# Kernel optimization log

Hardware: AMD Instinct MI355X
Metric: run time of the kernel (lower is better)

## Reference

```python
import jax, jax.numpy as jnp
import numpy as np

NUM_HEADS = 8  # from init_kwargs


def setup_inputs() -> dict:
    key = jax.random.key(0)
    ks = jax.random.split(key, 6)
    B, C, H, W = 16, 512, 64, 64
    ctx_dim = 256
    return {
        "x": jax.random.normal(ks[0], (B, C, H, W), dtype=jnp.float32),
        "context": jax.random.normal(ks[1], (B, ctx_dim), dtype=jnp.float32),
        "Wq": jax.random.normal(ks[2], (C, C), dtype=jnp.float32) * 0.02,
        "Wkv": jax.random.normal(ks[3], (2 * C, ctx_dim), dtype=jnp.float32) * 0.02,
        "Wout": jax.random.normal(ks[4], (C, C), dtype=jnp.float32) * 0.02,
        "bout": jax.random.normal(ks[5], (C,), dtype=jnp.float32) * 0.02,
    }


def reference(x, context, Wq, Wkv, Wout, bout):
    # x: [B, C, H, W], context: [B, ctx_dim]; single KV token cross-attention.
    B, C, H, W = x.shape
    N = H * W
    h = NUM_HEADS
    hd = C // h
    scale = hd ** -0.5

    xq = x.reshape(B, C, N).transpose(0, 2, 1)        # [B, N, C]
    q = xq @ Wq.T                                      # [B, N, C]
    kv = context @ Wkv.T                               # [B, 2C]
    k, v = kv[:, :C], kv[:, C:]                        # [B, C] each

    qh = q.reshape(B, N, h, hd)                        # [B, N, h, hd]
    kh = k.reshape(B, h, hd)                           # [B, h, hd] (single token)
    vh = v.reshape(B, h, hd)                           # [B, h, hd]

    # scores over a single KV token -> softmax over size-1 axis is all ones,
    # but we keep the faithful math as the correctness baseline.
    logits = jnp.einsum('bnhd,bhd->bnh', qh, kh) * scale   # [B, N, h]
    attn = jax.nn.softmax(logits[..., None], axis=-1)      # [B, N, h, 1]
    out = attn * vh[:, None, :, :]                         # [B, N, h, hd]
    out = out.reshape(B, N, C)

    out = out @ Wout.T + bout                              # to_out (dropout=identity)
    return out.transpose(0, 2, 1).reshape(B, C, H, W)
```

## Files before the change

### kernel.cpp

```cpp
#include <hip/hip_runtime.h>


#define BB   16
#define CC   512
#define CTX  256
#define NN   4096

typedef float f32x4 __attribute__((ext_vector_type(4)));

__global__ __launch_bounds__(256) void v_kernel(
    const float* __restrict__ ctx,
    const float* __restrict__ Wkv,
    float* __restrict__ v)
{
    const int b    = blockIdx.y;
    const int g    = blockIdx.x;
    const int wave = threadIdx.x >> 6;
    const int lane = threadIdx.x & 63;

    const f32x4 cx = ((const f32x4*)(ctx + b * CTX))[lane];
    const int jbase = g * 64 + wave * 16;

    #pragma unroll 4
    for (int i = 0; i < 16; ++i) {
        const int j = jbase + i;
        const f32x4 wv = ((const f32x4*)(Wkv + (size_t)(CC + j) * CTX))[lane];
        float p = wv.x * cx.x + wv.y * cx.y + wv.z * cx.z + wv.w * cx.w;
        #pragma unroll
        for (int m = 32; m >= 1; m >>= 1) p += __shfl_xor(p, m);
        if (lane == 0) v[b * CC + j] = p;
    }
}

__global__ __launch_bounds__(256) void out_kernel(
    const float* __restrict__ v,
    const float* __restrict__ Wout,
    const float* __restrict__ bout,
    f32x4* __restrict__ out)
{
    const int wave = threadIdx.x >> 6;
    const int lane = threadIdx.x & 63;
    const int row  = blockIdx.x * 4 + wave;
    const int b    = row >> 9;
    const int c    = row & (CC - 1);

    const f32x4* vr = (const f32x4*)(v + (size_t)b * CC);
    const f32x4* wr = (const f32x4*)(Wout + (size_t)c * CC);
    const f32x4 w0 = wr[lane],      v0 = vr[lane];
    const f32x4 w1 = wr[64 + lane], v1 = vr[64 + lane];

    float p = w0.x * v0.x + w0.y * v0.y + w0.z * v0.z + w0.w * v0.w
            + w1.x * v1.x + w1.y * v1.y + w1.z * v1.z + w1.w * v1.w;
    #pragma unroll
    for (int m = 32; m >= 1; m >>= 1) p += __shfl_xor(p, m);

    const float y = p + bout[c];
    f32x4 val;  val.x = y; val.y = y; val.z = y; val.w = y;

    f32x4* dst = out + (size_t)row * (NN / 4) + lane;
    #pragma unroll
    for (int j = 0; j < 16; ++j)
        dst[j * 64] = val;
}

extern "C" void kernel_launch(void* const* d_in, const int* in_sizes, int n_in,
                              void* d_out, int out_size, void* d_ws, size_t ws_size,
                              hipStream_t stream) {
    const float* context = (const float*)d_in[1];
    const float* Wkv     = (const float*)d_in[3];
    const float* Wout    = (const float*)d_in[4];
    const float* bout    = (const float*)d_in[5];
    float* out = (float*)d_out;
    float* v   = (float*)d_ws;

    v_kernel<<<dim3(8, BB), 256, 0, stream>>>(context, Wkv, v);
    out_kernel<<<(BB * CC) / 4, 256, 0, stream>>>(v, Wout, bout, (f32x4*)out);
}
```

Before: 34.65 us.

## Fuse V projection and output projection into one kernel with redundant V

```diff
diff --git a/kernel.cpp b/kernel.cpp
--- a/kernel.cpp
+++ b/kernel.cpp
@@ -8,59 +8,63 @@
 
 typedef float f32x4 __attribute__((ext_vector_type(4)));
 
-__global__ __launch_bounds__(256) void v_kernel(
+__global__ __launch_bounds__(512) void fused_kernel(
     const float* __restrict__ ctx,
     const float* __restrict__ Wkv,
-    float* __restrict__ v)
+    const float* __restrict__ Wout,
+    const float* __restrict__ bout,
+    f32x4* __restrict__ out)
 {
-    const int b    = blockIdx.y;
-    const int g    = blockIdx.x;
+    __shared__ float v_s[CC];
+    __shared__ float y_s[32];
+
     const int wave = threadIdx.x >> 6;
     const int lane = threadIdx.x & 63;
+    const int blk  = blockIdx.x;
+    const int b    = blk >> 4;
+    const int r0   = blk << 5;
+    const int c0   = (blk & 15) << 5;
 
     const f32x4 cx = ((const f32x4*)(ctx + b * CTX))[lane];
-    const int jbase = g * 64 + wave * 16;
 
+    const int j0 = wave << 6;
     #pragma unroll 4
-    for (int i = 0; i < 16; ++i) {
-        const int j = jbase + i;
+    for (int jj = 0; jj < 64; ++jj) {
+        const int j = j0 + jj;
         const f32x4 wv = ((const f32x4*)(Wkv + (size_t)(CC + j) * CTX))[lane];
         float p = wv.x * cx.x + wv.y * cx.y + wv.z * cx.z + wv.w * cx.w;
         #pragma unroll
         for (int m = 32; m >= 1; m >>= 1) p += __shfl_xor(p, m);
-        if (lane == 0) v[b * CC + j] = p;
+        if (lane == 0) v_s[j] = p;
     }
-}
+    __syncthreads();
 
-__global__ __launch_bounds__(256) void out_kernel(
-    const float* __restrict__ v,
-    const float* __restrict__ Wout,
-    const float* __restrict__ bout,
-    f32x4* __restrict__ out)
-{
-    const int wave = threadIdx.x >> 6;
-    const int lane = threadIdx.x & 63;
-    const int row  = blockIdx.x * 4 + wave;
-    const int b    = row >> 9;
-    const int c    = row & (CC - 1);
+    const f32x4* vr = (const f32x4*)v_s;
+    #pragma unroll
+    for (int i = 0; i < 4; ++i) {
+        const int cl = (wave << 2) + i;
+        const int c  = c0 + cl;
+        const f32x4* wr = (const f32x4*)(Wout + (size_t)c * CC);
+        const f32x4 w0 = wr[lane],      v0 = vr[lane];
+        const f32x4 w1 = wr[64 + lane], v1 = vr[64 + lane];
+        float p = w0.x * v0.x + w0.y * v0.y + w0.z * v0.z + w0.w * v0.w
+                + w1.x * v1.x + w1.y * v1.y + w1.z * v1.z + w1.w * v1.w;
+        #pragma unroll
+        for (int m = 32; m >= 1; m >>= 1) p += __shfl_xor(p, m);
+        if (lane == 0) y_s[cl] = p + bout[c];
+    }
+    __syncthreads();
 
-    const f32x4* vr = (const f32x4*)(v + (size_t)b * CC);
-    const f32x4* wr = (const f32x4*)(Wout + (size_t)c * CC);
-    const f32x4 w0 = wr[lane],      v0 = vr[lane];
-    const f32x4 w1 = wr[64 + lane], v1 = vr[64 + lane];
-
-    float p = w0.x * v0.x + w0.y * v0.y + w0.z * v0.z + w0.w * v0.w
-            + w1.x * v1.x + w1.y * v1.y + w1.z * v1.z + w1.w * v1.w;
     #pragma unroll
-    for (int m = 32; m >= 1; m >>= 1) p += __shfl_xor(p, m);
-
-    const float y = p + bout[c];
-    f32x4 val;  val.x = y; val.y = y; val.z = y; val.w = y;
-
-    f32x4* dst = out + (size_t)row * (NN / 4) + lane;
-    #pragma unroll
-    for (int j = 0; j < 16; ++j)
-        dst[j * 64] = val;
+    for (int i = 0; i < 4; ++i) {
+        const int cl = (wave << 2) + i;
+        const float yv = y_s[cl];
+        f32x4 val; val.x = yv; val.y = yv; val.z = yv; val.w = yv;
+        f32x4* dst = out + (size_t)(r0 + cl) * (NN / 4) + lane;
+        #pragma unroll
+        for (int j = 0; j < 16; ++j)
+            dst[j * 64] = val;
+    }
 }
 
 extern "C" void kernel_launch(void* const* d_in, const int* in_sizes, int n_in,
@@ -70,9 +74,7 @@
     const float* Wkv     = (const float*)d_in[3];
     const float* Wout    = (const float*)d_in[4];
     const float* bout    = (const float*)d_in[5];
-    float* out = (float*)d_out;
-    float* v   = (float*)d_ws;
+    f32x4* out = (f32x4*)d_out;
 
-    v_kernel<<<dim3(8, BB), 256, 0, stream>>>(context, Wkv, v);
-    out_kernel<<<(BB * CC) / 4, 256, 0, stream>>>(v, Wout, bout, (f32x4*)out);
+    fused_kernel<<<256, 512, 0, stream>>>(context, Wkv, Wout, bout, out);
 }
```

Measured after the change: 57.44 us. +65.8%, slower.

## Flatten v_kernel to one row per wave and reuse Wout rows across batches

Applied to the files above, without the earlier changes.

```diff
diff --git a/kernel.cpp b/kernel.cpp
--- a/kernel.cpp
+++ b/kernel.cpp
@@ -13,23 +13,17 @@
     const float* __restrict__ Wkv,
     float* __restrict__ v)
 {
-    const int b    = blockIdx.y;
-    const int g    = blockIdx.x;
-    const int wave = threadIdx.x >> 6;
+    const int w    = (blockIdx.x << 2) + (threadIdx.x >> 6);
     const int lane = threadIdx.x & 63;
+    const int b    = w >> 9;
+    const int j    = w & (CC - 1);
 
     const f32x4 cx = ((const f32x4*)(ctx + b * CTX))[lane];
-    const int jbase = g * 64 + wave * 16;
-
-    #pragma unroll 4
-    for (int i = 0; i < 16; ++i) {
-        const int j = jbase + i;
-        const f32x4 wv = ((const f32x4*)(Wkv + (size_t)(CC + j) * CTX))[lane];
-        float p = wv.x * cx.x + wv.y * cx.y + wv.z * cx.z + wv.w * cx.w;
-        #pragma unroll
-        for (int m = 32; m >= 1; m >>= 1) p += __shfl_xor(p, m);
-        if (lane == 0) v[b * CC + j] = p;
-    }
+    const f32x4 wv = ((const f32x4*)(Wkv + (size_t)(CC + j) * CTX))[lane];
+    float p = wv.x * cx.x + wv.y * cx.y + wv.z * cx.z + wv.w * cx.w;
+    #pragma unroll
+    for (int m = 32; m >= 1; m >>= 1) p += __shfl_xor(p, m);
+    if (lane == 0) v[w] = p;
 }
 
 __global__ __launch_bounds__(256) void out_kernel(
@@ -38,29 +32,36 @@
     const float* __restrict__ bout,
     f32x4* __restrict__ out)
 {
-    const int wave = threadIdx.x >> 6;
+    const int wid  = (blockIdx.x << 2) + (threadIdx.x >> 6);
     const int lane = threadIdx.x & 63;
-    const int row  = blockIdx.x * 4 + wave;
-    const int b    = row >> 9;
-    const int c    = row & (CC - 1);
+    const int c    = wid >> 1;
+    const int b0   = (wid & 1) << 3;
 
-    const f32x4* vr = (const f32x4*)(v + (size_t)b * CC);
     const f32x4* wr = (const f32x4*)(Wout + (size_t)c * CC);
-    const f32x4 w0 = wr[lane],      v0 = vr[lane];
-    const f32x4 w1 = wr[64 + lane], v1 = vr[64 + lane];
+    const f32x4 w0 = wr[lane], w1 = wr[64 + lane];
+    const float bb = bout[c];
 
-    float p = w0.x * v0.x + w0.y * v0.y + w0.z * v0.z + w0.w * v0.w
-            + w1.x * v1.x + w1.y * v1.y + w1.z * v1.z + w1.w * v1.w;
+    float yv[8];
     #pragma unroll
-    for (int m = 32; m >= 1; m >>= 1) p += __shfl_xor(p, m);
+    for (int i = 0; i < 8; ++i) {
+        const f32x4* vr = (const f32x4*)(v + (size_t)(b0 + i) * CC);
+        const f32x4 v0 = vr[lane], v1 = vr[64 + lane];
+        float p = w0.x * v0.x + w0.y * v0.y + w0.z * v0.z + w0.w * v0.w
+                + w1.x * v1.x + w1.y * v1.y + w1.z * v1.z + w1.w * v1.w;
+        #pragma unroll
+        for (int m = 32; m >= 1; m >>= 1) p += __shfl_xor(p, m);
+        yv[i] = p + bb;
+    }
 
-    const float y = p + bout[c];
-    f32x4 val;  val.x = y; val.y = y; val.z = y; val.w = y;
-
-    f32x4* dst = out + (size_t)row * (NN / 4) + lane;
     #pragma unroll
-    for (int j = 0; j < 16; ++j)
-        dst[j * 64] = val;
+    for (int i = 0; i < 8; ++i) {
+        const int row = ((b0 + i) << 9) + c;
+        f32x4 val; val.x = yv[i]; val.y = yv[i]; val.z = yv[i]; val.w = yv[i];
+        f32x4* dst = out + (size_t)row * (NN / 4) + lane;
+        #pragma unroll
+        for (int j = 0; j < 16; ++j)
+            dst[j * 64] = val;
+    }
 }
 
 extern "C" void kernel_launch(void* const* d_in, const int* in_sizes, int n_in,
@@ -70,9 +71,9 @@
     const float* Wkv     = (const float*)d_in[3];
     const float* Wout    = (const float*)d_in[4];
     const float* bout    = (const float*)d_in[5];
-    float* out = (float*)d_out;
+    f32x4* out = (f32x4*)d_out;
     float* v   = (float*)d_ws;
 
-    v_kernel<<<dim3(8, BB), 256, 0, stream>>>(context, Wkv, v);
-    out_kernel<<<(BB * CC) / 4, 256, 0, stream>>>(v, Wout, bout, (f32x4*)out);
+    v_kernel<<<2048, 256, 0, stream>>>(context, Wkv, v);
+    out_kernel<<<256, 256, 0, stream>>>(v, Wout, bout, out);
 }
```

After: 31.52 us. -9.0%, faster.
